# Performance work log

Measured on AMD Instinct MI355X. Metric: run time of the kernel, lower is better.

Reference implementation:

```python
import jax, jax.numpy as jnp
import numpy as np

B, C, W, H = 16, 256, 32, 32
HEADS = 4


def setup_inputs() -> dict:
    key = jax.random.key(0)
    ks = jax.random.split(key, 9)
    d = C // HEADS
    return {
        "x": jax.random.normal(ks[0], (B, C, W, H), jnp.float32),
        "Wq": jax.random.normal(ks[1], (C, C), jnp.float32) * 0.05,
        "bq": jax.random.normal(ks[2], (C,), jnp.float32) * 0.05,
        "Wk": jax.random.normal(ks[3], (C, C), jnp.float32) * 0.05,
        "bk": jax.random.normal(ks[4], (C,), jnp.float32) * 0.05,
        "Wv": jax.random.normal(ks[5], (C, C), jnp.float32) * 0.05,
        "bv": jax.random.normal(ks[6], (C,), jnp.float32) * 0.05,
        "rel_h": jax.random.normal(ks[7], (1, HEADS, d, 1, H), jnp.float32),
        "rel_w": jax.random.normal(ks[8], (1, HEADS, d, W, 1), jnp.float32),
    }


def reference(x, Wq, bq, Wk, bk, Wv, bv, rel_h, rel_w):
    b, c, w, h = x.shape
    heads = rel_h.shape[1]
    d = c // heads
    n = w * h  # sequence length = spatial positions
    xf = x.reshape(b, c, n)

    def proj(Wt, bt):
        # 1x1 conv == per-position linear over channels
        y = jnp.einsum('oc,bcn->bon', Wt, xf) + bt[None, :, None]
        return y.reshape(b, heads, d, n)

    q = proj(Wq, bq)
    k = proj(Wk, bk)
    v = proj(Wv, bv)

    # similarity = q^T k : [b, heads, n, n]
    sim = jnp.einsum('bhdi,bhdj->bhij', q, k)
    # relative position bias content term: rel^T q
    rel = (rel_h + rel_w).reshape(heads, d, n)  # broadcast-add then flatten spatial
    qpos = jnp.einsum('hdi,bhdj->bhij', rel, q)

    attn = jax.nn.softmax(sim + qpos, axis=-1)
    # out = v @ attn^T : [b, heads, d, n]
    out = jnp.einsum('bhdn,bhmn->bhdm', v, attn)
    return out.reshape(b, c, w, h)
```

## Files before the change

kernel.cpp:

```cpp
#include <hip/hip_runtime.h>

constexpr int Bb  = 16;
constexpr int Cch = 256;
constexpr int NH  = 4;
constexpr int Dh  = 64;
constexpr int Nn  = 1024;

typedef _Float16 f16;
typedef __attribute__((ext_vector_type(8))) _Float16 f16x8;
typedef __attribute__((ext_vector_type(4))) _Float16 f16x4;
typedef __attribute__((ext_vector_type(4))) float    f32x4;

__global__ __launch_bounds__(256) void prep_kernel(
    const float* __restrict__ x,
    const float* __restrict__ Wq, const float* __restrict__ Wk,
    const float* __restrict__ Wv,
    const float* __restrict__ rel_h, const float* __restrict__ rel_w,
    f16* __restrict__ xt, f16* __restrict__ Wh, f16* __restrict__ rel_t)
{
    const int gx = blockIdx.x;
    const int t  = threadIdx.x;
    __shared__ float T[64][65];

    if (gx < 1024) {
        const int n0 = (gx & 15) * 64;
        const int c0 = ((gx >> 4) & 3) * 64;
        const int b  = gx >> 6;
        #pragma unroll
        for (int rep = 0; rep < 16; rep++) {
            const int e  = t + rep * 256;
            const int r  = e >> 6;
            const int cc = e & 63;
            T[r][cc] = x[((size_t)b * Cch + c0 + r) * Nn + n0 + cc];
        }
        __syncthreads();
        #pragma unroll
        for (int rep = 0; rep < 4; rep++) {
            const int e  = t + rep * 256;
            const int nn = e >> 4;
            const int c4 = e & 15;
            f16x4 w;
            w.x = (f16)T[c4 * 4 + 0][nn];
            w.y = (f16)T[c4 * 4 + 1][nn];
            w.z = (f16)T[c4 * 4 + 2][nn];
            w.w = (f16)T[c4 * 4 + 3][nn];
            *(f16x4*)&xt[((size_t)b * Nn + n0 + nn) * Cch + c0 + c4 * 4] = w;
        }
    } else if (gx < 2048) {
        const int idx = (gx - 1024) * 256 + t;
        const int d = idx & 63;
        const int n = (idx >> 6) & (Nn - 1);
        const int h = idx >> 16;
        const int hd = h * 64 + d;
        rel_t[idx] = (f16)(rel_h[hd * 32 + (n & 31)] + rel_w[hd * 32 + (n >> 5)]);
    } else {
        const int idx = (gx - 2048) * 256 + t;
        const int og  = idx >> 8;
        const int c   = idx & 255;
        const int p   = og >> 8;
        const int o   = og & 255;
        const float* W = (p == 0) ? Wq : (p == 1) ? Wk : Wv;
        Wh[idx] = (f16)W[o * 256 + c];
    }
}

__global__ __launch_bounds__(256) void gemm_qkv(
    const f16* __restrict__ Wh, const f16* __restrict__ xt,
    const float* __restrict__ bq, const float* __restrict__ bk,
    const float* __restrict__ bv,
    f16* __restrict__ qt, f16* __restrict__ kt, f16* __restrict__ vb)
{
    const int bx   = blockIdx.x;
    const int y    = blockIdx.y;
    const int b    = blockIdx.z;
    const int p    = y >> 1;
    const int half = y & 1;

    constexpr int ST = 40;
    __shared__ f16 Wt[128 * ST];
    __shared__ f16 Xt[128 * ST];

    const int t    = threadIdx.x;
    const int wave = t >> 6;
    const int lane = t & 63;
    const int l16  = lane & 15;
    const int quad = lane >> 4;
    const int wm   = wave >> 1;
    const int wsd  = wave & 1;

    f32x4 acc[4][4];
    #pragma unroll
    for (int mi = 0; mi < 4; mi++)
        #pragma unroll
        for (int ni = 0; ni < 4; ni++) acc[mi][ni] = (f32x4){0.f, 0.f, 0.f, 0.f};

    const f16* Wg = Wh + (size_t)y * 128 * 256;
    const f16* Xg = xt + ((size_t)b * Nn + bx * 128) * 256;

    for (int c0 = 0; c0 < 256; c0 += 32) {
        f16x8 wch[2], xch[2];
        #pragma unroll
        for (int rep = 0; rep < 2; rep++) {
            const int e   = t + rep * 256;
            const int row = e >> 2;
            const int c8  = e & 3;
            wch[rep] = *(const f16x8*)&Wg[(size_t)row * 256 + c0 + c8 * 8];
            xch[rep] = *(const f16x8*)&Xg[(size_t)row * 256 + c0 + c8 * 8];
        }
        __syncthreads();
        #pragma unroll
        for (int rep = 0; rep < 2; rep++) {
            const int e   = t + rep * 256;
            const int row = e >> 2;
            const int c8  = e & 3;
            *(f16x8*)&Wt[row * ST + c8 * 8] = wch[rep];
            *(f16x8*)&Xt[row * ST + c8 * 8] = xch[rep];
        }
        __syncthreads();

        const f16* tf = (p < 2) ? Wt : Xt;
        const f16* ts = (p < 2) ? Xt : Wt;
        f16x8 af[4], bf[4];
        #pragma unroll
        for (int mi = 0; mi < 4; mi++)
            af[mi] = *(const f16x8*)&tf[(wm * 64 + mi * 16 + l16) * ST + quad * 8];
        #pragma unroll
        for (int ni = 0; ni < 4; ni++)
            bf[ni] = *(const f16x8*)&ts[(wsd * 64 + ni * 16 + l16) * ST + quad * 8];
        #pragma unroll
        for (int mi = 0; mi < 4; mi++)
            #pragma unroll
            for (int ni = 0; ni < 4; ni++)
                acc[mi][ni] = __builtin_amdgcn_mfma_f32_16x16x32_f16(
                    af[mi], bf[ni], acc[mi][ni], 0, 0, 0);
    }

    if (p < 2) {
        f16* yt = (p == 0) ? qt : kt;
        const float* bg = (p == 0) ? bq : bk;
        #pragma unroll
        for (int mi = 0; mi < 4; mi++) {
            const int o_in = half * 128 + wm * 64 + mi * 16 + quad * 4;
            const float4 b4 = *(const float4*)&bg[o_in];
            const int h = o_in >> 6;
            const int d = o_in & 63;
            #pragma unroll
            for (int ni = 0; ni < 4; ni++) {
                const int n = bx * 128 + wsd * 64 + ni * 16 + l16;
                f16x4 w;
                w.x = (f16)(acc[mi][ni][0] + b4.x);
                w.y = (f16)(acc[mi][ni][1] + b4.y);
                w.z = (f16)(acc[mi][ni][2] + b4.z);
                w.w = (f16)(acc[mi][ni][3] + b4.w);
                *(f16x4*)&yt[(((size_t)b * NH + h) * Nn + n) * Dh + d] = w;
            }
        }
    } else {
        #pragma unroll
        for (int ni = 0; ni < 4; ni++) {
            const int c  = half * 128 + wsd * 64 + ni * 16 + l16;
            const float bs = bv[c];
            #pragma unroll
            for (int mi = 0; mi < 4; mi++) {
                const int n = bx * 128 + wm * 64 + mi * 16 + quad * 4;
                f16x4 w;
                w.x = (f16)(acc[mi][ni][0] + bs);
                w.y = (f16)(acc[mi][ni][1] + bs);
                w.z = (f16)(acc[mi][ni][2] + bs);
                w.w = (f16)(acc[mi][ni][3] + bs);
                *(f16x4*)&vb[((size_t)b * Cch + c) * Nn + n] = w;
            }
        }
    }
}

__global__ __launch_bounds__(256, 2) void attn_mfma(
    const f16* __restrict__ qt, const f16* __restrict__ kt,
    const f16* __restrict__ relt, const f16* __restrict__ vb,
    float* __restrict__ out)
{
    const int i0 = blockIdx.x * 128;
    const int h  = blockIdx.y;
    const int b  = blockIdx.z;
    const int bh = b * NH + h;

    const f16* qtb = qt  + (size_t)bh * Nn * Dh;
    const f16* ktb = kt  + (size_t)bh * Nn * Dh;
    const f16* rlt = relt + (size_t)h * Nn * Dh;
    const f16* vbb = vb  + (size_t)(b * Cch + h * Dh) * Nn;

    __shared__ f16 Qa_s[128 * 128];
    __shared__ f16 Ka_s[64 * 128];
    __shared__ f16 v_s [64 * 64];
    __shared__ f16 Pt_s[128 * 64];

    const int t    = threadIdx.x;
    const int wave = t >> 6;
    const int lane = t & 63;
    const int l16  = lane & 15;
    const int quad = lane >> 4;

    #pragma unroll
    for (int rep = 0; rep < 8; rep++) {
        const int e   = t + rep * 256;
        const int row = e >> 4;
        const int c8  = e & 15;
        const f16* src = (c8 < 8)
            ? &qtb[(size_t)(i0 + row) * Dh + c8 * 8]
            : &rlt[(size_t)(i0 + row) * Dh + (c8 - 8) * 8];
        *(f16x8*)&Qa_s[(row << 7) + ((c8 ^ (row & 7)) << 3)] = *(const f16x8*)src;
    }
    __syncthreads();

    f16x8 af[2][4];
    #pragma unroll
    for (int ms = 0; ms < 2; ms++) {
        const int row = wave * 32 + ms * 16 + l16;
        #pragma unroll
        for (int k = 0; k < 4; k++)
            af[ms][k] = *(const f16x8*)
                &Qa_s[(row << 7) + ((((k << 2) + quad) ^ (row & 7)) << 3)];
    }

    f16x8 ones;
    #pragma unroll
    for (int u = 0; u < 8; u++) ones[u] = (f16)1.0f;

    f32x4 Of[2][4], Ol[2];
    float m_r[2][4];
    #pragma unroll
    for (int ms = 0; ms < 2; ms++) {
        Ol[ms] = (f32x4){0.f, 0.f, 0.f, 0.f};
        #pragma unroll
        for (int ds = 0; ds < 4; ds++) Of[ms][ds] = (f32x4){0.f, 0.f, 0.f, 0.f};
        #pragma unroll
        for (int r = 0; r < 4; r++) m_r[ms][r] = -1e30f;
    }

    for (int j0 = 0; j0 < Nn; j0 += 64) {
        f16x8 kreg[4], vreg[2];
        #pragma unroll
        for (int rep = 0; rep < 4; rep++) {
            const int e   = t + rep * 256;
            const int row = e >> 4;
            const int c8  = e & 15;
            const f16* src = (c8 < 8)
                ? &ktb[(size_t)(j0 + row) * Dh + c8 * 8]
                : &qtb[(size_t)(j0 + row) * Dh + (c8 - 8) * 8];
            kreg[rep] = *(const f16x8*)src;
        }
        #pragma unroll
        for (int rep = 0; rep < 2; rep++) {
            const int e   = t + rep * 256;
            const int row = e >> 3;
            const int c8  = e & 7;
            vreg[rep] = *(const f16x8*)&vbb[(size_t)row * Nn + j0 + c8 * 8];
        }

        __syncthreads();
        #pragma unroll
        for (int rep = 0; rep < 4; rep++) {
            const int e   = t + rep * 256;
            const int row = e >> 4;
            const int c8  = e & 15;
            *(f16x8*)&Ka_s[(row << 7) + ((c8 ^ (row & 7)) << 3)] = kreg[rep];
        }
        #pragma unroll
        for (int rep = 0; rep < 2; rep++) {
            const int e   = t + rep * 256;
            const int row = e >> 3;
            const int c8  = e & 7;
            *(f16x8*)&v_s[(row << 6) + ((c8 ^ (row & 7)) << 3)] = vreg[rep];
        }
        __syncthreads();

        f32x4 Sf[2][4];
        #pragma unroll
        for (int ms = 0; ms < 2; ms++)
            #pragma unroll
            for (int js = 0; js < 4; js++) Sf[ms][js] = (f32x4){0.f, 0.f, 0.f, 0.f};
        #pragma unroll
        for (int k = 0; k < 4; k++) {
            f16x8 bb[4];
            #pragma unroll
            for (int js = 0; js < 4; js++) {
                const int row = js * 16 + l16;
                bb[js] = *(const f16x8*)
                    &Ka_s[(row << 7) + ((((k << 2) + quad) ^ (row & 7)) << 3)];
            }
            #pragma unroll
            for (int ms = 0; ms < 2; ms++)
                #pragma unroll
                for (int js = 0; js < 4; js++)
                    Sf[ms][js] = __builtin_amdgcn_mfma_f32_16x16x32_f16(
                        af[ms][k], bb[js], Sf[ms][js], 0, 0, 0);
        }

        #pragma unroll
        for (int ms = 0; ms < 2; ms++) {
            #pragma unroll
            for (int r = 0; r < 4; r++) {
                float tm = fmaxf(fmaxf(Sf[ms][0][r], Sf[ms][1][r]),
                                 fmaxf(Sf[ms][2][r], Sf[ms][3][r]));
                tm = fmaxf(tm, __shfl_xor(tm, 1));
                tm = fmaxf(tm, __shfl_xor(tm, 2));
                tm = fmaxf(tm, __shfl_xor(tm, 4));
                tm = fmaxf(tm, __shfl_xor(tm, 8));
                const float mnew  = fmaxf(m_r[ms][r], tm);
                const float alpha = __expf(m_r[ms][r] - mnew);
                m_r[ms][r] = mnew;

                const int row = wave * 32 + ms * 16 + quad * 4 + r;
                const int rx  = row & 7;
                #pragma unroll
                for (int js = 0; js < 4; js++) {
                    const float p = __expf(Sf[ms][js][r] - mnew);
                    const int col = js * 16 + l16;
                    Pt_s[(row << 6) + (((col >> 3) ^ rx) << 3) + (col & 7)] = (f16)p;
                }
                #pragma unroll
                for (int ds = 0; ds < 4; ds++) Of[ms][ds][r] *= alpha;
                Ol[ms][r] *= alpha;
            }
        }

        #pragma unroll
        for (int ks = 0; ks < 2; ks++) {
            #pragma unroll
            for (int ms = 0; ms < 2; ms++) {
                const int prow = wave * 32 + ms * 16 + l16;
                f16x8 pa = *(const f16x8*)
                    &Pt_s[(prow << 6) + ((((ks << 2) + quad) ^ (prow & 7)) << 3)];
                #pragma unroll
                for (int ds = 0; ds < 4; ds++) {
                    const int vrow = ds * 16 + l16;
                    f16x8 vv = *(const f16x8*)
                        &v_s[(vrow << 6) + ((((ks << 2) + quad) ^ (vrow & 7)) << 3)];
                    Of[ms][ds] = __builtin_amdgcn_mfma_f32_16x16x32_f16(
                        pa, vv, Of[ms][ds], 0, 0, 0);
                }
                Ol[ms] = __builtin_amdgcn_mfma_f32_16x16x32_f16(
                    pa, ones, Ol[ms], 0, 0, 0);
            }
        }
    }

    #pragma unroll
    for (int ms = 0; ms < 2; ms++) {
        #pragma unroll
        for (int r = 0; r < 4; r++) {
            const float inv = 1.0f / Ol[ms][r];
            const int i = i0 + wave * 32 + ms * 16 + quad * 4 + r;
            #pragma unroll
            for (int ds = 0; ds < 4; ds++) {
                const int d = ds * 16 + l16;
                out[((size_t)(b * Cch + h * Dh + d)) * Nn + i] = Of[ms][ds][r] * inv;
            }
        }
    }
}

extern "C" void kernel_launch(void* const* d_in, const int* in_sizes, int n_in,
                              void* d_out, int out_size, void* d_ws, size_t ws_size,
                              hipStream_t stream)
{
    const float* x     = (const float*)d_in[0];
    const float* Wq    = (const float*)d_in[1];
    const float* bq    = (const float*)d_in[2];
    const float* Wk    = (const float*)d_in[3];
    const float* bk    = (const float*)d_in[4];
    const float* Wv    = (const float*)d_in[5];
    const float* bv    = (const float*)d_in[6];
    const float* rel_h = (const float*)d_in[7];
    const float* rel_w = (const float*)d_in[8];

    f16* ws = (f16*)d_ws;
    const size_t SZQ = (size_t)Bb * NH * Nn * Dh;
    f16* qt   = ws;
    f16* kt   = ws + SZQ;
    f16* vbuf = ws + 2 * SZQ;
    f16* relt = ws + 3 * SZQ;
    f16* xth  = ws + 3 * SZQ + (size_t)NH * Nn * Dh;
    f16* Wh   = xth + SZQ;

    prep_kernel<<<dim3(2816), 256, 0, stream>>>(
        x, Wq, Wk, Wv, rel_h, rel_w, xth, Wh, relt);
    gemm_qkv<<<dim3(Nn / 128, 6, Bb), 256, 0, stream>>>(
        Wh, xth, bq, bk, bv, qt, kt, vbuf);
    attn_mfma<<<dim3(Nn / 128, NH, Bb), 256, 0, stream>>>(
        qt, kt, relt, vbuf, (float*)d_out);
}
```

Baseline: 157.6 us.

## Use direct global-to-LDS loads, exp2 softmax, smaller attention tiles

Both GEMM and attention kernels now stage tiles with global_load_lds instead of register round-trips, using XOR-swizzled layouts. The QKV GEMM takes a 64-wide K step. The attention kernel shrinks to 64 query rows per block (16 per wave), loads Q/rel fragments straight into registers, and runs at higher occupancy with a flattened grid that groups blocks by batch-head. LOG2E is folded into K and rel during preprocessing so softmax can use exp2f. Smaller query tiles raise occupancy and cut LDS use, but each K/V tile is now reused by fewer query rows, so global traffic goes up.

Measured after the change: 161.4 us. 2.4% more time.

```diff
diff --git a/kernel.cpp b/kernel.cpp
--- a/kernel.cpp
+++ b/kernel.cpp
@@ -10,6 +10,15 @@
 typedef __attribute__((ext_vector_type(8))) _Float16 f16x8;
 typedef __attribute__((ext_vector_type(4))) _Float16 f16x4;
 typedef __attribute__((ext_vector_type(4))) float    f32x4;
+
+#define LOG2E 1.44269504088896f
+
+__device__ inline void gld16(const f16* g, const f16* lds_wave_base) {
+    __builtin_amdgcn_global_load_lds(
+        (const __attribute__((address_space(1))) unsigned int*)g,
+        (__attribute__((address_space(3))) unsigned int*)lds_wave_base,
+        16, 0, 0);
+}
 
 __global__ __launch_bounds__(256) void prep_kernel(
     const float* __restrict__ x,
@@ -52,7 +61,8 @@
         const int n = (idx >> 6) & (Nn - 1);
         const int h = idx >> 16;
         const int hd = h * 64 + d;
-        rel_t[idx] = (f16)(rel_h[hd * 32 + (n & 31)] + rel_w[hd * 32 + (n >> 5)]);
+        rel_t[idx] = (f16)((rel_h[hd * 32 + (n & 31)] + rel_w[hd * 32 + (n >> 5)])
+                           * LOG2E);
     } else {
         const int idx = (gx - 2048) * 256 + t;
         const int og  = idx >> 8;
@@ -64,7 +74,7 @@
     }
 }
 
-__global__ __launch_bounds__(256) void gemm_qkv(
+__global__ __launch_bounds__(256, 3) void gemm_qkv(
     const f16* __restrict__ Wh, const f16* __restrict__ xt,
     const float* __restrict__ bq, const float* __restrict__ bk,
     const float* __restrict__ bv,
@@ -76,9 +86,8 @@
     const int p    = y >> 1;
     const int half = y & 1;
 
-    constexpr int ST = 40;
-    __shared__ f16 Wt[128 * ST];
-    __shared__ f16 Xt[128 * ST];
+    __shared__ f16 Wt[128 * 64];
+    __shared__ f16 Xt[128 * 64];
 
     const int t    = threadIdx.x;
     const int wave = t >> 6;
@@ -97,44 +106,53 @@
     const f16* Wg = Wh + (size_t)y * 128 * 256;
     const f16* Xg = xt + ((size_t)b * Nn + bx * 128) * 256;
 
-    for (int c0 = 0; c0 < 256; c0 += 32) {
-        f16x8 wch[2], xch[2];
-        #pragma unroll
-        for (int rep = 0; rep < 2; rep++) {
+    for (int c0 = 0; c0 < 256; c0 += 64) {
+        __syncthreads();
+        #pragma unroll
+        for (int rep = 0; rep < 4; rep++) {
             const int e   = t + rep * 256;
-            const int row = e >> 2;
-            const int c8  = e & 3;
-            wch[rep] = *(const f16x8*)&Wg[(size_t)row * 256 + c0 + c8 * 8];
-            xch[rep] = *(const f16x8*)&Xg[(size_t)row * 256 + c0 + c8 * 8];
-        }
-        __syncthreads();
-        #pragma unroll
-        for (int rep = 0; rep < 2; rep++) {
+            const int row = e >> 3;
+            const int c8s = (e & 7) ^ (row & 7);
+            gld16(&Wg[(size_t)row * 256 + c0 + c8s * 8],
+                  &Wt[((size_t)rep * 256 + wave * 64) * 8]);
+        }
+        #pragma unroll
+        for (int rep = 0; rep < 4; rep++) {
             const int e   = t + rep * 256;
-            const int row = e >> 2;
-            const int c8  = e & 3;
-            *(f16x8*)&Wt[row * ST + c8 * 8] = wch[rep];
-            *(f16x8*)&Xt[row * ST + c8 * 8] = xch[rep];
+            const int row = e >> 3;
+            const int c8s = (e & 7) ^ (row & 7);
+            gld16(&Xg[(size_t)row * 256 + c0 + c8s * 8],
+                  &Xt[((size_t)rep * 256 + wave * 64) * 8]);
         }
         __syncthreads();
 
         const f16* tf = (p < 2) ? Wt : Xt;
         const f16* ts = (p < 2) ? Xt : Wt;
-        f16x8 af[4], bf[4];
-        #pragma unroll
-        for (int mi = 0; mi < 4; mi++)
-            af[mi] = *(const f16x8*)&tf[(wm * 64 + mi * 16 + l16) * ST + quad * 8];
-        #pragma unroll
-        for (int ni = 0; ni < 4; ni++)
-            bf[ni] = *(const f16x8*)&ts[(wsd * 64 + ni * 16 + l16) * ST + quad * 8];
-        #pragma unroll
-        for (int mi = 0; mi < 4; mi++)
-            #pragma unroll
-            for (int ni = 0; ni < 4; ni++)
-                acc[mi][ni] = __builtin_amdgcn_mfma_f32_16x16x32_f16(
-                    af[mi], bf[ni], acc[mi][ni], 0, 0, 0);
-    }
-
+        #pragma unroll
+        for (int kk = 0; kk < 2; kk++) {
+            f16x8 af[4], bf[4];
+            #pragma unroll
+            for (int mi = 0; mi < 4; mi++) {
+                const int row = wm * 64 + mi * 16 + l16;
+                af[mi] = *(const f16x8*)
+                    &tf[row * 64 + (((kk * 4 + quad) ^ (row & 7)) << 3)];
+            }
+            #pragma unroll
+            for (int ni = 0; ni < 4; ni++) {
+                const int row = wsd * 64 + ni * 16 + l16;
+                bf[ni] = *(const f16x8*)
+                    &ts[row * 64 + (((kk * 4 + quad) ^ (row & 7)) << 3)];
+            }
+            #pragma unroll
+            for (int mi = 0; mi < 4; mi++)
+                #pragma unroll
+                for (int ni = 0; ni < 4; ni++)
+                    acc[mi][ni] = __builtin_amdgcn_mfma_f32_16x16x32_f16(
+                        af[mi], bf[ni], acc[mi][ni], 0, 0, 0);
+        }
+    }
+
+    const float scale = (p == 1) ? LOG2E : 1.0f;
     if (p < 2) {
         f16* yt = (p == 0) ? qt : kt;
         const float* bg = (p == 0) ? bq : bk;
@@ -148,10 +166,10 @@
             for (int ni = 0; ni < 4; ni++) {
                 const int n = bx * 128 + wsd * 64 + ni * 16 + l16;
                 f16x4 w;
-                w.x = (f16)(acc[mi][ni][0] + b4.x);
-                w.y = (f16)(acc[mi][ni][1] + b4.y);
-                w.z = (f16)(acc[mi][ni][2] + b4.z);
-                w.w = (f16)(acc[mi][ni][3] + b4.w);
+                w.x = (f16)((acc[mi][ni][0] + b4.x) * scale);
+                w.y = (f16)((acc[mi][ni][1] + b4.y) * scale);
+                w.z = (f16)((acc[mi][ni][2] + b4.z) * scale);
+                w.w = (f16)((acc[mi][ni][3] + b4.w) * scale);
                 *(f16x4*)&yt[(((size_t)b * NH + h) * Nn + n) * Dh + d] = w;
             }
         }
@@ -174,25 +192,25 @@
     }
 }
 
-__global__ __launch_bounds__(256, 2) void attn_mfma(
+__global__ __launch_bounds__(256, 4) void attn_mfma(
     const f16* __restrict__ qt, const f16* __restrict__ kt,
     const f16* __restrict__ relt, const f16* __restrict__ vb,
     float* __restrict__ out)
 {
-    const int i0 = blockIdx.x * 128;
-    const int h  = blockIdx.y;
-    const int b  = blockIdx.z;
-    const int bh = b * NH + h;
+    const int g  = blockIdx.x;
+    const int bh = g & 63;
+    const int i0 = (g >> 6) * 64;
+    const int b  = bh >> 2;
+    const int h  = bh & 3;
 
     const f16* qtb = qt  + (size_t)bh * Nn * Dh;
     const f16* ktb = kt  + (size_t)bh * Nn * Dh;
     const f16* rlt = relt + (size_t)h * Nn * Dh;
     const f16* vbb = vb  + (size_t)(b * Cch + h * Dh) * Nn;
 
-    __shared__ f16 Qa_s[128 * 128];
     __shared__ f16 Ka_s[64 * 128];
     __shared__ f16 v_s [64 * 64];
-    __shared__ f16 Pt_s[128 * 64];
+    __shared__ f16 Pt_s[64 * 64];
 
     const int t    = threadIdx.x;
     const int wave = t >> 6;
@@ -200,85 +218,50 @@
     const int l16  = lane & 15;
     const int quad = lane >> 4;
 
-    #pragma unroll
-    for (int rep = 0; rep < 8; rep++) {
-        const int e   = t + rep * 256;
-        const int row = e >> 4;
-        const int c8  = e & 15;
-        const f16* src = (c8 < 8)
-            ? &qtb[(size_t)(i0 + row) * Dh + c8 * 8]
-            : &rlt[(size_t)(i0 + row) * Dh + (c8 - 8) * 8];
-        *(f16x8*)&Qa_s[(row << 7) + ((c8 ^ (row & 7)) << 3)] = *(const f16x8*)src;
-    }
-    __syncthreads();
-
-    f16x8 af[2][4];
-    #pragma unroll
-    for (int ms = 0; ms < 2; ms++) {
-        const int row = wave * 32 + ms * 16 + l16;
-        #pragma unroll
-        for (int k = 0; k < 4; k++)
-            af[ms][k] = *(const f16x8*)
-                &Qa_s[(row << 7) + ((((k << 2) + quad) ^ (row & 7)) << 3)];
-    }
+    const int arow = i0 + wave * 16 + l16;
+    f16x8 af[4];
+    af[0] = *(const f16x8*)&qtb[(size_t)arow * Dh + quad * 8];
+    af[1] = *(const f16x8*)&qtb[(size_t)arow * Dh + 32 + quad * 8];
+    af[2] = *(const f16x8*)&rlt[(size_t)arow * Dh + quad * 8];
+    af[3] = *(const f16x8*)&rlt[(size_t)arow * Dh + 32 + quad * 8];
 
     f16x8 ones;
     #pragma unroll
     for (int u = 0; u < 8; u++) ones[u] = (f16)1.0f;
 
-    f32x4 Of[2][4], Ol[2];
-    float m_r[2][4];
-    #pragma unroll
-    for (int ms = 0; ms < 2; ms++) {
-        Ol[ms] = (f32x4){0.f, 0.f, 0.f, 0.f};
-        #pragma unroll
-        for (int ds = 0; ds < 4; ds++) Of[ms][ds] = (f32x4){0.f, 0.f, 0.f, 0.f};
-        #pragma unroll
-        for (int r = 0; r < 4; r++) m_r[ms][r] = -1e30f;
-    }
+    f32x4 Of[4], Ol;
+    Ol = (f32x4){0.f, 0.f, 0.f, 0.f};
+    #pragma unroll
+    for (int ds = 0; ds < 4; ds++) Of[ds] = (f32x4){0.f, 0.f, 0.f, 0.f};
+    float m_r[4];
+    #pragma unroll
+    for (int r = 0; r < 4; r++) m_r[r] = -1e30f;
 
     for (int j0 = 0; j0 < Nn; j0 += 64) {
-        f16x8 kreg[4], vreg[2];
+        __syncthreads();
         #pragma unroll
         for (int rep = 0; rep < 4; rep++) {
             const int e   = t + rep * 256;
             const int row = e >> 4;
-            const int c8  = e & 15;
-            const f16* src = (c8 < 8)
-                ? &ktb[(size_t)(j0 + row) * Dh + c8 * 8]
-                : &qtb[(size_t)(j0 + row) * Dh + (c8 - 8) * 8];
-            kreg[rep] = *(const f16x8*)src;
+            const int c8s = (e & 15) ^ (row & 7);
+            const f16* src = (c8s < 8)
+                ? &ktb[(size_t)(j0 + row) * Dh + c8s * 8]
+                : &qtb[(size_t)(j0 + row) * Dh + (c8s - 8) * 8];
+            gld16(src, &Ka_s[((size_t)rep * 256 + wave * 64) * 8]);
         }
         #pragma unroll
         for (int rep = 0; rep < 2; rep++) {
             const int e   = t + rep * 256;
             const int row = e >> 3;
-            const int c8  = e & 7;
-            vreg[rep] = *(const f16x8*)&vbb[(size_t)row * Nn + j0 + c8 * 8];
-        }
-
-        __syncthreads();
-        #pragma unroll
-        for (int rep = 0; rep < 4; rep++) {
-            const int e   = t + rep * 256;
-            const int row = e >> 4;
-            const int c8  = e & 15;
-            *(f16x8*)&Ka_s[(row << 7) + ((c8 ^ (row & 7)) << 3)] = kreg[rep];
-        }
-        #pragma unroll
-        for (int rep = 0; rep < 2; rep++) {
-            const int e   = t + rep * 256;
-            const int row = e >> 3;
-            const int c8  = e & 7;
-            *(f16x8*)&v_s[(row << 6) + ((c8 ^ (row & 7)) << 3)] = vreg[rep];
-        }
-        __syncthreads();
-
-        f32x4 Sf[2][4];
-        #pragma unroll
-        for (int ms = 0; ms < 2; ms++)
-            #pragma unroll
-            for (int js = 0; js < 4; js++) Sf[ms][js] = (f32x4){0.f, 0.f, 0.f, 0.f};
+            const int c8s = (e & 7) ^ (row & 7);
+            gld16(&vbb[(size_t)row * Nn + j0 + c8s * 8],
+                  &v_s[((size_t)rep * 256 + wave * 64) * 8]);
+        }
+        __syncthreads();
+
+        f32x4 Sf[4];
+        #pragma unroll
+        for (int js = 0; js < 4; js++) Sf[js] = (f32x4){0.f, 0.f, 0.f, 0.f};
         #pragma unroll
         for (int k = 0; k < 4; k++) {
             f16x8 bb[4];
@@ -286,76 +269,63 @@
             for (int js = 0; js < 4; js++) {
                 const int row = js * 16 + l16;
                 bb[js] = *(const f16x8*)
-                    &Ka_s[(row << 7) + ((((k << 2) + quad) ^ (row & 7)) << 3)];
-            }
-            #pragma unroll
-            for (int ms = 0; ms < 2; ms++)
-                #pragma unroll
-                for (int js = 0; js < 4; js++)
-                    Sf[ms][js] = __builtin_amdgcn_mfma_f32_16x16x32_f16(
-                        af[ms][k], bb[js], Sf[ms][js], 0, 0, 0);
-        }
-
-        #pragma unroll
-        for (int ms = 0; ms < 2; ms++) {
-            #pragma unroll
-            for (int r = 0; r < 4; r++) {
-                float tm = fmaxf(fmaxf(Sf[ms][0][r], Sf[ms][1][r]),
-                                 fmaxf(Sf[ms][2][r], Sf[ms][3][r]));
-                tm = fmaxf(tm, __shfl_xor(tm, 1));
-                tm = fmaxf(tm, __shfl_xor(tm, 2));
-                tm = fmaxf(tm, __shfl_xor(tm, 4));
-                tm = fmaxf(tm, __shfl_xor(tm, 8));
-                const float mnew  = fmaxf(m_r[ms][r], tm);
-                const float alpha = __expf(m_r[ms][r] - mnew);
-                m_r[ms][r] = mnew;
-
-                const int row = wave * 32 + ms * 16 + quad * 4 + r;
-                const int rx  = row & 7;
-                #pragma unroll
-                for (int js = 0; js < 4; js++) {
-                    const float p = __expf(Sf[ms][js][r] - mnew);
-                    const int col = js * 16 + l16;
-                    Pt_s[(row << 6) + (((col >> 3) ^ rx) << 3) + (col & 7)] = (f16)p;
-                }
-                #pragma unroll
-                for (int ds = 0; ds < 4; ds++) Of[ms][ds][r] *= alpha;
-                Ol[ms][r] *= alpha;
-            }
+                    &Ka_s[row * 128 + (((k * 4 + quad) ^ (row & 7)) << 3)];
+            }
+            #pragma unroll
+            for (int js = 0; js < 4; js++)
+                Sf[js] = __builtin_amdgcn_mfma_f32_16x16x32_f16(
+                    af[k], bb[js], Sf[js], 0, 0, 0);
+        }
+
+        #pragma unroll
+        for (int r = 0; r < 4; r++) {
+            float tm = fmaxf(fmaxf(Sf[0][r], Sf[1][r]), fmaxf(Sf[2][r], Sf[3][r]));
+            tm = fmaxf(tm, __shfl_xor(tm, 1));
+            tm = fmaxf(tm, __shfl_xor(tm, 2));
+            tm = fmaxf(tm, __shfl_xor(tm, 4));
+            tm = fmaxf(tm, __shfl_xor(tm, 8));
+            const float mnew  = fmaxf(m_r[r], tm);
+            const float alpha = exp2f(m_r[r] - mnew);
+            m_r[r] = mnew;
+
+            const int row = wave * 16 + quad * 4 + r;
+            const int rx  = row & 7;
+            #pragma unroll
+            for (int js = 0; js < 4; js++) {
+                const float p = exp2f(Sf[js][r] - mnew);
+                const int col = js * 16 + l16;
+                Pt_s[row * 64 + (((col >> 3) ^ rx) << 3) + (col & 7)] = (f16)p;
+            }
+            #pragma unroll
+            for (int ds = 0; ds < 4; ds++) Of[ds][r] *= alpha;
+            Ol[r] *= alpha;
         }
 
         #pragma unroll
         for (int ks = 0; ks < 2; ks++) {
-            #pragma unroll
-            for (int ms = 0; ms < 2; ms++) {
-                const int prow = wave * 32 + ms * 16 + l16;
-                f16x8 pa = *(const f16x8*)
-                    &Pt_s[(prow << 6) + ((((ks << 2) + quad) ^ (prow & 7)) << 3)];
-                #pragma unroll
-                for (int ds = 0; ds < 4; ds++) {
-                    const int vrow = ds * 16 + l16;
-                    f16x8 vv = *(const f16x8*)
-                        &v_s[(vrow << 6) + ((((ks << 2) + quad) ^ (vrow & 7)) << 3)];
-                    Of[ms][ds] = __builtin_amdgcn_mfma_f32_16x16x32_f16(
-                        pa, vv, Of[ms][ds], 0, 0, 0);
-                }
-                Ol[ms] = __builtin_amdgcn_mfma_f32_16x16x32_f16(
-                    pa, ones, Ol[ms], 0, 0, 0);
-            }
-        }
-    }
-
-    #pragma unroll
-    for (int ms = 0; ms < 2; ms++) {
-        #pragma unroll
-        for (int r = 0; r < 4; r++) {
-            const float inv = 1.0f / Ol[ms][r];
-            const int i = i0 + wave * 32 + ms * 16 + quad * 4 + r;
+            const int prow = wave * 16 + l16;
+            f16x8 pa = *(const f16x8*)
+                &Pt_s[prow * 64 + (((ks * 4 + quad) ^ (prow & 7)) << 3)];
             #pragma unroll
             for (int ds = 0; ds < 4; ds++) {
-                const int d = ds * 16 + l16;
-                out[((size_t)(b * Cch + h * Dh + d)) * Nn + i] = Of[ms][ds][r] * inv;
-            }
+                const int vrow = ds * 16 + l16;
+                f16x8 vv = *(const f16x8*)
+                    &v_s[vrow * 64 + (((ks * 4 + quad) ^ (vrow & 7)) << 3)];
+                Of[ds] = __builtin_amdgcn_mfma_f32_16x16x32_f16(
+                    pa, vv, Of[ds], 0, 0, 0);
+            }
+            Ol = __builtin_amdgcn_mfma_f32_16x16x32_f16(pa, ones, Ol, 0, 0, 0);
+        }
+    }
+
+    #pragma unroll
+    for (int r = 0; r < 4; r++) {
+        const float inv = 1.0f / Ol[r];
+        const int i = i0 + wave * 16 + quad * 4 + r;
+        #pragma unroll
+        for (int ds = 0; ds < 4; ds++) {
+            const int d = ds * 16 + l16;
+            out[((size_t)(b * Cch + h * Dh + d)) * Nn + i] = Of[ds][r] * inv;
         }
     }
 }
@@ -387,6 +357,6 @@
         x, Wq, Wk, Wv, rel_h, rel_w, xth, Wh, relt);
     gemm_qkv<<<dim3(Nn / 128, 6, Bb), 256, 0, stream>>>(
         Wh, xth, bq, bk, bv, qt, kt, vbuf);
-    attn_mfma<<<dim3(Nn / 128, NH, Bb), 256, 0, stream>>>(
+    attn_mfma<<<dim3(64 * (Nn / 64)), 256, 0, stream>>>(
         qt, kt, relt, vbuf, (float*)d_out);
 }
```
